# Performance work log

Hardware: AMD Instinct MI355X
Metric: run time of the kernel (lower is better)

The kernel has to match this reference:

```python
import jax, jax.numpy as jnp
import numpy as np

NHEAD = 8
HB, WB = 16, 16  # block_size


def _mha(q, k, v, w_in, b_in, w_out, b_out, nhead):
    # q,k,v: [L, B, C] seq-first, like torch.nn.MultiheadAttention (eval mode, no dropout)
    Lq, B, C = q.shape
    d = C // nhead
    wq, wk, wv = jnp.split(w_in, 3, axis=0)
    bq, bk, bv = jnp.split(b_in, 3)
    qh = (q @ wq.T + bq).reshape(Lq, B, nhead, d).transpose(1, 2, 0, 3)        # [B,H,Lq,d]
    kh = (k @ wk.T + bk).reshape(k.shape[0], B, nhead, d).transpose(1, 2, 0, 3)
    vh = (v @ wv.T + bv).reshape(v.shape[0], B, nhead, d).transpose(1, 2, 0, 3)
    scale = 1.0 / jnp.sqrt(jnp.asarray(d, dtype=qh.dtype))
    scores = jnp.einsum('bhqd,bhkd->bhqk', qh * scale, kh)
    attn = jax.nn.softmax(scores, axis=-1)
    out = jnp.einsum('bhqk,bhkd->bhqd', attn, vh)                               # [B,H,Lq,d]
    out = out.transpose(2, 0, 1, 3).reshape(Lq, B, C)
    return out @ w_out.T + b_out


def setup_inputs() -> dict:
    key = jax.random.key(0)
    ks = jax.random.split(key, 12)
    n, c, t, h, w = 2, 256, 2, 64, 64
    q = jax.random.normal(ks[0], (n, c, t, h, w), dtype=jnp.float32)
    k = jax.random.normal(ks[1], (n, c, t, h, w), dtype=jnp.float32)
    v = jax.random.normal(ks[2], (n, c, t, h, w), dtype=jnp.float32)
    pos = jax.random.normal(ks[3], (n, c, t, h, w), dtype=jnp.float32)
    s = 0.02
    wl_in = jax.random.normal(ks[4], (3 * c, c), dtype=jnp.float32) * s
    bl_in = jnp.zeros((3 * c,), dtype=jnp.float32)
    wl_out = jax.random.normal(ks[5], (c, c), dtype=jnp.float32) * s
    bl_out = jnp.zeros((c,), dtype=jnp.float32)
    ws_in = jax.random.normal(ks[6], (3 * c, c), dtype=jnp.float32) * s
    bs_in = jnp.zeros((3 * c,), dtype=jnp.float32)
    ws_out = jax.random.normal(ks[7], (c, c), dtype=jnp.float32) * s
    bs_out = jnp.zeros((c,), dtype=jnp.float32)
    return {"q": q, "k": k, "v": v, "pos": pos,
            "wl_in": wl_in, "bl_in": bl_in, "wl_out": wl_out, "bl_out": bl_out,
            "ws_in": ws_in, "bs_in": bs_in, "ws_out": ws_out, "bs_out": bs_out}


def reference(q, k, v, pos, wl_in, bl_in, wl_out, bl_out, ws_in, bs_in, ws_out, bs_out):
    n, c, t_q, h, w = q.shape
    t_k = k.shape[2]
    bn_h, bn_w = h // HB, w // WB

    def to_long(x, t):
        # [n,c,t,h,w] -> [t*bn_h*bn_w, n*HB*WB, c]
        x = x.reshape(n, c, t, bn_h, HB, bn_w, WB).transpose(2, 3, 5, 0, 4, 6, 1)
        return x.reshape(t * bn_h * bn_w, n * HB * WB, c)

    ql = to_long(q, t_q)
    kl = to_long(k, t_k)
    vl = to_long(v, t_k)
    pl = to_long(pos, t_q)

    v1 = _mha(ql + pl, kl + pl, vl, wl_in, bl_in, wl_out, bl_out, NHEAD)

    def long_to_short(x):
        # [t*bn_h*bn_w, n*HB*WB, c] -> [t*HB*WB, n*bn_h*bn_w, c]
        x = x.reshape(t_q, bn_h, bn_w, n, HB, WB, c).transpose(0, 4, 5, 3, 1, 2, 6)
        return x.reshape(t_q * HB * WB, n * bn_h * bn_w, c)

    v2 = long_to_short(v1)
    ps = long_to_short(pl)

    out = _mha(v2 + ps, v2 + ps, v2, ws_in, bs_in, ws_out, bs_out, NHEAD)
    out = out.reshape(t_q, HB, WB, n, bn_h, bn_w, c).transpose(3, 6, 0, 4, 1, 5, 2)
    return out.reshape(n, c, t_q, h, w)
```

## Files before the change

kernel.cpp:

```cpp
#include <hip/hip_runtime.h>
#include <math.h>


#define SCALE_D32 0.17677669529663687f
#define EXP2_SCALE 0.25508680987930193f
#define GLOBAL_AS __attribute__((address_space(1)))
#define LDS_AS __attribute__((address_space(3)))

typedef short short8 __attribute__((ext_vector_type(8)));
typedef short short4v __attribute__((ext_vector_type(4)));
typedef short short2v __attribute__((ext_vector_type(2)));
typedef float floatx4 __attribute__((ext_vector_type(4)));

__device__ __forceinline__ short f2bf(float f) {
  union { float f; unsigned u; } x;
  x.f = f;
  unsigned r = x.u + 0x7fffu + ((x.u >> 16) & 1u);
  return (short)(r >> 16);
}
__device__ __forceinline__ float bf2f(short s) {
  union { unsigned u; float f; } x;
  x.u = ((unsigned)(unsigned short)s) << 16;
  return x.f;
}

__global__ __launch_bounds__(256) void pack_kernel(
    const float* __restrict__ q, const float* __restrict__ k,
    const float* __restrict__ v, const float* __restrict__ pos,
    short* __restrict__ Xp, short* __restrict__ Xq,
    short* __restrict__ Xk, short* __restrict__ Xv,
    const float* __restrict__ wl_in, const float* __restrict__ wl_out,
    const float* __restrict__ ws_in, const float* __restrict__ ws_out,
    short* __restrict__ wbf) {
  __shared__ float tP[64][65];
  __shared__ float tX[64][65];
  int b = blockIdx.x;
  int cb = b & 3;
  int h  = (b >> 2) & 63;
  int nt = b >> 8;
  int n = nt >> 1, t = nt & 1;
  int c0 = cb * 64;
  int bh = h >> 4, ii = h & 15;
  long inbase = (long)n * 2097152 + (long)t * 4096 + (long)h * 64;
  int tx = threadIdx.x & 63;
  int ty = threadIdx.x >> 6;

  for (int cc = ty; cc < 64; cc += 4) {
    long a = inbase + (long)(c0 + cc) * 8192 + tx;
    tP[cc][tx] = pos[a];
    tX[cc][tx] = q[a];
  }
  __syncthreads();
  for (int ww = ty; ww < 64; ww += 4) {
    int bw = ww >> 4, j = ww & 15;
    int m1 = (((t * 4 + bh) * 4 + bw) * 512) + n * 256 + ii * 16 + j;
    long o = (long)m1 * 256 + c0 + tx;
    float pv = tP[tx][ww];
    Xp[o] = f2bf(pv);
    Xq[o] = f2bf(tX[tx][ww] + pv);
  }
  __syncthreads();
  for (int cc = ty; cc < 64; cc += 4) {
    long a = inbase + (long)(c0 + cc) * 8192 + tx;
    tX[cc][tx] = k[a];
  }
  __syncthreads();
  for (int ww = ty; ww < 64; ww += 4) {
    int bw = ww >> 4, j = ww & 15;
    int m1 = (((t * 4 + bh) * 4 + bw) * 512) + n * 256 + ii * 16 + j;
    long o = (long)m1 * 256 + c0 + tx;
    Xk[o] = f2bf(tX[tx][ww] + tP[tx][ww]);
  }
  __syncthreads();
  for (int cc = ty; cc < 64; cc += 4) {
    long a = inbase + (long)(c0 + cc) * 8192 + tx;
    tX[cc][tx] = v[a];
  }
  __syncthreads();
  for (int ww = ty; ww < 64; ww += 4) {
    int bw = ww >> 4, j = ww & 15;
    int m1 = (((t * 4 + bh) * 4 + bw) * 512) + n * 256 + ii * 16 + j;
    long o = (long)m1 * 256 + c0 + tx;
    Xv[o] = f2bf(tX[tx][ww]);
  }
  int idx = (blockIdx.x * 256 + threadIdx.x) * 2;
  const float* wp;
  if (idx < 196608) wp = wl_in + idx;
  else if (idx < 262144) wp = wl_out + (idx - 196608);
  else if (idx < 458752) wp = ws_in + (idx - 262144);
  else wp = ws_out + (idx - 458752);
  float2 wv = *(const float2*)wp;
  wbf[idx] = f2bf(wv.x);
  wbf[idx + 1] = f2bf(wv.y);
}

template <bool OUT32>
__global__ __launch_bounds__(256) void gemm_tri(
    const short* __restrict__ A0, const short* __restrict__ A1,
    const short* __restrict__ A2, const short* __restrict__ W0,
    const float* __restrict__ bias0, void* __restrict__ C0,
    void* __restrict__ C1, void* __restrict__ C2) {
  __shared__ short As[128 * 64];
  __shared__ short Ws[64 * 64];
  int z = blockIdx.z;
  const short* A = (z == 0) ? A0 : ((z == 1) ? A1 : A2);
  const short* Wb = W0 + z * 65536;
  const float* bias = bias0 + z * 256;
  void* Csel = (z == 0) ? C0 : ((z == 1) ? C1 : C2);
  int m0 = blockIdx.x * 128;
  int n0 = blockIdx.y * 64;
  int tid = threadIdx.x;
  int lane = tid & 63, wave = tid >> 6;
  int wm = wave >> 1, wn = wave & 1;
  int l15 = lane & 15, quad = lane >> 4;
  int x7 = l15 & 7;
  int rsub = lane >> 3;
  int csub = lane & 7;

  floatx4 acc[4][2];
#pragma unroll
  for (int mt = 0; mt < 4; ++mt)
#pragma unroll
    for (int nt = 0; nt < 2; ++nt) acc[mt][nt] = (floatx4)(0.f);

  for (int kb = 0; kb < 4; ++kb) {
    int k0 = kb * 64;
    if (kb) __syncthreads();
#pragma unroll
    for (int j = 0; j < 4; ++j) {
      int r0 = (wave * 4 + j) * 8;
      int row = r0 + rsub;
      int c = csub ^ (row & 7);
      const short* gp = A + (long)(m0 + row) * 256 + k0 + c * 8;
      short* lp = &As[r0 * 64 + lane * 8];
      __builtin_amdgcn_global_load_lds((const GLOBAL_AS void*)gp,
                                       (LDS_AS void*)lp, 16, 0, 0);
    }
#pragma unroll
    for (int j = 0; j < 2; ++j) {
      int r0 = (wave * 2 + j) * 8;
      int row = r0 + rsub;
      int c = csub ^ (row & 7);
      const short* gp = Wb + (long)(n0 + row) * 256 + k0 + c * 8;
      short* lp = &Ws[r0 * 64 + lane * 8];
      __builtin_amdgcn_global_load_lds((const GLOBAL_AS void*)gp,
                                       (LDS_AS void*)lp, 16, 0, 0);
    }
    __syncthreads();
#pragma unroll
    for (int ks = 0; ks < 2; ++ks) {
      int pc = (ks * 4 + quad) ^ x7;
      short8 af[4], bfr[2];
#pragma unroll
      for (int mt = 0; mt < 4; ++mt) {
        int row = wm * 64 + mt * 16 + l15;
        af[mt] = *(const short8*)&As[row * 64 + pc * 8];
      }
#pragma unroll
      for (int nt = 0; nt < 2; ++nt) {
        int row = wn * 32 + nt * 16 + l15;
        bfr[nt] = *(const short8*)&Ws[row * 64 + pc * 8];
      }
#pragma unroll
      for (int mt = 0; mt < 4; ++mt)
#pragma unroll
        for (int nt = 0; nt < 2; ++nt)
          acc[mt][nt] = __builtin_amdgcn_mfma_f32_16x16x32_bf16(
              af[mt], bfr[nt], acc[mt][nt], 0, 0, 0);
    }
  }
  float bia0 = bias[n0 + wn * 32 + l15];
  float bia1 = bias[n0 + wn * 32 + 16 + l15];
#pragma unroll
  for (int mt = 0; mt < 4; ++mt) {
#pragma unroll
    for (int r = 0; r < 4; ++r) {
      int row = m0 + wm * 64 + mt * 16 + quad * 4 + r;
      long base = (long)row * 256 + n0 + wn * 32 + l15;
      if (OUT32) {
        float* C = (float*)Csel;
        C[base] = acc[mt][0][r] + bia0;
        C[base + 16] = acc[mt][1][r] + bia1;
      } else {
        short* C = (short*)Csel;
        C[base] = f2bf(acc[mt][0][r] + bia0);
        C[base + 16] = f2bf(acc[mt][1][r] + bia1);
      }
    }
  }
}

__global__ __launch_bounds__(256) void attn1_mfma(
    const short* __restrict__ Q1, const short* __restrict__ K1,
    const short* __restrict__ V1, short* __restrict__ O1) {
  __shared__ short Vs[32][264];
  __shared__ short Vt[4][32][40];
  __shared__ short Pw[4][32][40];
  int b1 = blockIdx.x;
  int tid = threadIdx.x;
  int wave = tid >> 6, lane = tid & 63;
  int l15 = lane & 15, quad = lane >> 4;

#pragma unroll
  for (int p = 0; p < 4; ++p) {
    int idx = p * 256 + tid;
    int row = idx >> 5;
    int c8 = idx & 31;
    *(short8*)&Vs[row][c8 * 8] =
        *(const short8*)(V1 + ((long)row * 512 + b1) * 256 + c8 * 8);
  }
  __syncthreads();

  int key = lane & 31;
  int dh = (lane >> 5) * 16;
  int pc = 2 * (key & 15) + (key >> 4);

#pragma unroll
  for (int h2 = 0; h2 < 2; ++h2) {
    int hh = wave * 2 + h2;
    long fbase = ((long)l15 * 512 + b1) * 256 + hh * 32 + quad * 8;
    short8 qf0 = *(const short8*)(Q1 + fbase);
    short8 qf1 = *(const short8*)(Q1 + fbase + 16 * 512 * 256);
    short8 kf0 = *(const short8*)(K1 + fbase);
    short8 kf1 = *(const short8*)(K1 + fbase + 16 * 512 * 256);
    short8 v0 = *(const short8*)&Vs[key][hh * 32 + dh];
    short8 v1 = *(const short8*)&Vs[key][hh * 32 + dh + 8];
#pragma unroll
    for (int j = 0; j < 8; ++j) {
      Vt[wave][dh + j][pc] = v0[j];
      Vt[wave][dh + 8 + j][pc] = v1[j];
    }
    floatx4 s00 = __builtin_amdgcn_mfma_f32_16x16x32_bf16(qf0, kf0, (floatx4)(0.f), 0, 0, 0);
    floatx4 s01 = __builtin_amdgcn_mfma_f32_16x16x32_bf16(qf0, kf1, (floatx4)(0.f), 0, 0, 0);
    floatx4 s10 = __builtin_amdgcn_mfma_f32_16x16x32_bf16(qf1, kf0, (floatx4)(0.f), 0, 0, 0);
    floatx4 s11 = __builtin_amdgcn_mfma_f32_16x16x32_bf16(qf1, kf1, (floatx4)(0.f), 0, 0, 0);
    float li0[4], li1[4];
#pragma unroll
    for (int r = 0; r < 4; ++r) {
      float p00 = __builtin_amdgcn_exp2f(s00[r] * EXP2_SCALE);
      float p01 = __builtin_amdgcn_exp2f(s01[r] * EXP2_SCALE);
      float p10 = __builtin_amdgcn_exp2f(s10[r] * EXP2_SCALE);
      float p11 = __builtin_amdgcn_exp2f(s11[r] * EXP2_SCALE);
      li0[r] = p00 + p01;
      li1[r] = p10 + p11;
      short2v pa, pb;
      pa.x = f2bf(p00); pa.y = f2bf(p01);
      pb.x = f2bf(p10); pb.y = f2bf(p11);
      *(short2v*)&Pw[wave][quad * 4 + r][2 * l15] = pa;
      *(short2v*)&Pw[wave][16 + quad * 4 + r][2 * l15] = pb;
    }
#pragma unroll
    for (int r = 0; r < 4; ++r) {
      li0[r] += __shfl_xor(li0[r], 1, 64);
      li0[r] += __shfl_xor(li0[r], 2, 64);
      li0[r] += __shfl_xor(li0[r], 4, 64);
      li0[r] += __shfl_xor(li0[r], 8, 64);
      li1[r] += __shfl_xor(li1[r], 1, 64);
      li1[r] += __shfl_xor(li1[r], 2, 64);
      li1[r] += __shfl_xor(li1[r], 4, 64);
      li1[r] += __shfl_xor(li1[r], 8, 64);
    }
    short8 pf0 = *(const short8*)&Pw[wave][l15][quad * 8];
    short8 pf1 = *(const short8*)&Pw[wave][16 + l15][quad * 8];
    short8 vt0 = *(const short8*)&Vt[wave][l15][quad * 8];
    short8 vt1 = *(const short8*)&Vt[wave][16 + l15][quad * 8];
    floatx4 o00 = __builtin_amdgcn_mfma_f32_16x16x32_bf16(pf0, vt0, (floatx4)(0.f), 0, 0, 0);
    floatx4 o01 = __builtin_amdgcn_mfma_f32_16x16x32_bf16(pf0, vt1, (floatx4)(0.f), 0, 0, 0);
    floatx4 o10 = __builtin_amdgcn_mfma_f32_16x16x32_bf16(pf1, vt0, (floatx4)(0.f), 0, 0, 0);
    floatx4 o11 = __builtin_amdgcn_mfma_f32_16x16x32_bf16(pf1, vt1, (floatx4)(0.f), 0, 0, 0);
#pragma unroll
    for (int r = 0; r < 4; ++r) {
      float inv0 = 1.f / li0[r];
      float inv1 = 1.f / li1[r];
      long oa = ((long)(quad * 4 + r) * 512 + b1) * 256 + hh * 32 + l15;
      long ob = ((long)(16 + quad * 4 + r) * 512 + b1) * 256 + hh * 32 + l15;
      O1[oa] = f2bf(o00[r] * inv0);
      O1[oa + 16] = f2bf(o01[r] * inv0);
      O1[ob] = f2bf(o10[r] * inv1);
      O1[ob + 16] = f2bf(o11[r] * inv1);
    }
  }
}

__global__ __launch_bounds__(256) void attn2_mfma(
    const short* __restrict__ Q2, const short* __restrict__ K2,
    const short* __restrict__ V2, short* __restrict__ O2) {
  __shared__ short Ks[64][40];
  __shared__ short Vt[32][72];
  __shared__ short Pw[4][16][72];
  int bid = blockIdx.x;
  int rest = bid & 255;
  int qblk = bid >> 8;
  int hh = 2 * (rest & 3) + (rest >> 7);
  int b2 = (rest >> 2) & 31;
  int tid = threadIdx.x;
  int wave = tid >> 6, lane = tid & 63;
  int l15 = lane & 15, quad = lane >> 4;

  short8 qf;
  {
    long tok = (long)(qblk * 64 + wave * 16 + l15) * 32 + b2;
    qf = *(const short8*)(Q2 + tok * 256 + hh * 32 + quad * 8);
  }
  floatx4 Oa = (floatx4)(0.f), Ob = (floatx4)(0.f);
  float li[4] = {0.f, 0.f, 0.f, 0.f};

  int skey = tid >> 2;
  int sd0 = (tid & 3) * 8;
  int vkey = lane;
  int vd0 = wave * 8;
  int vcol = (vkey & 15) * 4 + (vkey >> 4);

  for (int kb = 0; kb < 8; ++kb) {
    if (kb) __syncthreads();
    {
      long tok = (long)(kb * 64 + skey) * 32 + b2;
      *(short8*)&Ks[skey][sd0] = *(const short8*)(K2 + tok * 256 + hh * 32 + sd0);
    }
    {
      long tok = (long)(kb * 64 + vkey) * 32 + b2;
      short8 v = *(const short8*)(V2 + tok * 256 + hh * 32 + vd0);
#pragma unroll
      for (int j = 0; j < 8; ++j) Vt[vd0 + j][vcol] = v[j];
    }
    __syncthreads();
    floatx4 st[4];
#pragma unroll
    for (int kt = 0; kt < 4; ++kt) {
      short8 kf = *(const short8*)&Ks[kt * 16 + l15][quad * 8];
      st[kt] = __builtin_amdgcn_mfma_f32_16x16x32_bf16(qf, kf, (floatx4)(0.f), 0, 0, 0);
    }
#pragma unroll
    for (int r = 0; r < 4; ++r) {
      float p0 = __builtin_amdgcn_exp2f(st[0][r] * EXP2_SCALE);
      float p1 = __builtin_amdgcn_exp2f(st[1][r] * EXP2_SCALE);
      float p2 = __builtin_amdgcn_exp2f(st[2][r] * EXP2_SCALE);
      float p3 = __builtin_amdgcn_exp2f(st[3][r] * EXP2_SCALE);
      li[r] += (p0 + p1) + (p2 + p3);
      short4v pp;
      pp.x = f2bf(p0); pp.y = f2bf(p1); pp.z = f2bf(p2); pp.w = f2bf(p3);
      *(short4v*)&Pw[wave][quad * 4 + r][l15 * 4] = pp;
    }
#pragma unroll
    for (int kk = 0; kk < 2; ++kk) {
      short8 pf = *(const short8*)&Pw[wave][l15][kk * 32 + quad * 8];
      short8 v0 = *(const short8*)&Vt[l15][kk * 32 + quad * 8];
      short8 v1 = *(const short8*)&Vt[16 + l15][kk * 32 + quad * 8];
      Oa = __builtin_amdgcn_mfma_f32_16x16x32_bf16(pf, v0, Oa, 0, 0, 0);
      Ob = __builtin_amdgcn_mfma_f32_16x16x32_bf16(pf, v1, Ob, 0, 0, 0);
    }
  }
#pragma unroll
  for (int r = 0; r < 4; ++r) {
    float s = li[r];
    s += __shfl_xor(s, 1, 64);
    s += __shfl_xor(s, 2, 64);
    s += __shfl_xor(s, 4, 64);
    s += __shfl_xor(s, 8, 64);
    float inv = 1.f / s;
    long tok = (long)(qblk * 64 + wave * 16 + quad * 4 + r) * 32 + b2;
    long a = tok * 256 + hh * 32 + l15;
    O2[a] = f2bf(Oa[r] * inv);
    O2[a + 16] = f2bf(Ob[r] * inv);
  }
}

__global__ __launch_bounds__(256) void perm12_kernel(
    const short8* __restrict__ V1o, const short8* __restrict__ Xp,
    short8* __restrict__ X2, short8* __restrict__ V2in) {
  int gg = blockIdx.x * 256 + threadIdx.x;
  int m1 = gg >> 5, seg = gg & 31;
  int l1 = m1 >> 9, b1 = m1 & 511;
  int t = l1 >> 4, bh = (l1 >> 2) & 3, bw = l1 & 3;
  int n = b1 >> 8, ii = (b1 >> 4) & 15, j = b1 & 15;
  int l2 = t * 256 + ii * 16 + j;
  int b2 = n * 16 + bh * 4 + bw;
  int m2 = l2 * 32 + b2;
  short8 v = V1o[gg];
  short8 p = Xp[gg];
  short8 x;
#pragma unroll
  for (int jj = 0; jj < 8; ++jj) x[jj] = f2bf(bf2f(v[jj]) + bf2f(p[jj]));
  X2[m2 * 32 + seg] = x;
  V2in[m2 * 32 + seg] = v;
}

__global__ __launch_bounds__(256) void unpack_kernel(
    const float* __restrict__ Y, float* __restrict__ out) {
  __shared__ float tl[64][65];
  int b = blockIdx.x;
  int cb = b & 3;
  int h = (b >> 2) & 63;
  int nt = b >> 8;
  int n = nt >> 1, t = nt & 1;
  int c0 = cb * 64;
  int bh = h >> 4, ii = h & 15;
  int tx = threadIdx.x & 63;
  int ty = threadIdx.x >> 6;
  for (int ww = ty; ww < 64; ww += 4) {
    int bw = ww >> 4, j = ww & 15;
    int l2 = t * 256 + ii * 16 + j;
    int b2 = n * 16 + bh * 4 + bw;
    int m2 = l2 * 32 + b2;
    tl[tx][ww] = Y[(long)m2 * 256 + c0 + tx];
  }
  __syncthreads();
  long ob = (long)n * 2097152 + (long)t * 4096 + (long)h * 64 + tx;
  for (int cc = ty; cc < 64; cc += 4) {
    out[ob + (long)(c0 + cc) * 8192] = tl[cc][tx];
  }
}

extern "C" void kernel_launch(void* const* d_in, const int* in_sizes, int n_in,
                              void* d_out, int out_size, void* d_ws, size_t ws_size,
                              hipStream_t stream) {
  const float* q      = (const float*)d_in[0];
  const float* k      = (const float*)d_in[1];
  const float* v      = (const float*)d_in[2];
  const float* pos    = (const float*)d_in[3];
  const float* wl_in  = (const float*)d_in[4];
  const float* bl_in  = (const float*)d_in[5];
  const float* wl_out = (const float*)d_in[6];
  const float* bl_out = (const float*)d_in[7];
  const float* ws_in  = (const float*)d_in[8];
  const float* bs_in  = (const float*)d_in[9];
  const float* ws_out = (const float*)d_in[10];
  const float* bs_out = (const float*)d_in[11];
  float* out = (float*)d_out;
  char* wsb = (char*)d_ws;
  const size_t SLB = 16777216;
  short* s0 = (short*)(wsb);
  short* wbf = (short*)(wsb + SLB / 2);
  short* s1 = (short*)(wsb + SLB);
  short* s2 = (short*)(wsb + 2 * SLB);
  short* s3 = (short*)(wsb + 3 * SLB);
  short* s4 = (short*)(wsb + 4 * SLB);
  short* s5 = (short*)(wsb + 5 * SLB);
  short* s6 = (short*)(wsb + 6 * SLB);

  pack_kernel<<<1024, 256, 0, stream>>>(q, k, v, pos, s0, s1, s2, s3,
                                        wl_in, wl_out, ws_in, ws_out, wbf);

  dim3 g3(128, 4, 3);
  dim3 g1(128, 4, 1);
  gemm_tri<false><<<g3, 256, 0, stream>>>(s1, s2, s3, wbf, bl_in, s4, s5, s6);

  attn1_mfma<<<512, 256, 0, stream>>>(s4, s5, s6, s1);
  gemm_tri<false><<<g1, 256, 0, stream>>>(s1, s1, s1, wbf + 196608, bl_out,
                                          s2, s2, s2);

  perm12_kernel<<<2048, 256, 0, stream>>>((const short8*)s2, (const short8*)s0,
                                          (short8*)s3, (short8*)s4);

  gemm_tri<false><<<g3, 256, 0, stream>>>(s3, s3, s4, wbf + 262144, bs_in,
                                          s5, s6, s1);

  attn2_mfma<<<2048, 256, 0, stream>>>(s5, s6, s1, s3);
  gemm_tri<true><<<g1, 256, 0, stream>>>(s3, s3, s3, wbf + 458752, bs_out,
                                         s2, s2, s2);

  unpack_kernel<<<1024, 256, 0, stream>>>((const float*)s2, out);
}
```

Baseline: 221.4 us.

## Fuse first attention, its output projection and the long-to-short permute

The first attention kernel now keeps each block's 32x256 output tile in swizzled LDS and multiplies it by the out-projection weights, which are streamed into LDS with global_load_lds. It adds bias and pos and writes X2 and V2in straight into the short-sequence layout. This removes a GEMM launch, the permute kernel and two intermediate round trips through global memory. In exchange, each block redundantly reloads the full 256x256 weight matrix, the kernel uses more LDS, and the epilogue stores are scattered 2-byte writes rather than vectorised ones.

```diff
diff --git a/kernel.cpp b/kernel.cpp
--- a/kernel.cpp
+++ b/kernel.cpp
@@ -22,6 +22,10 @@
   union { unsigned u; float f; } x;
   x.u = ((unsigned)(unsigned short)s) << 16;
   return x.f;
+}
+
+__device__ __forceinline__ int o1s_phys(int q, int ch) {
+  return q * 256 + (ch & ~63) + ((((ch >> 3) & 7) ^ (q & 7)) << 3) + (ch & 7);
 }
 
 __global__ __launch_bounds__(256) void pack_kernel(
@@ -190,30 +194,46 @@
   }
 }
 
-__global__ __launch_bounds__(256) void attn1_mfma(
+__global__ __launch_bounds__(256) void attn1_fused(
     const short* __restrict__ Q1, const short* __restrict__ K1,
-    const short* __restrict__ V1, short* __restrict__ O1) {
-  __shared__ short Vs[32][264];
-  __shared__ short Vt[4][32][40];
-  __shared__ short Pw[4][32][40];
+    const short* __restrict__ V1, const short* __restrict__ Xp,
+    const short* __restrict__ Wo, const float* __restrict__ bias,
+    short* __restrict__ X2, short* __restrict__ V2in) {
+  __shared__ union {
+    struct {
+      short Vs[32][264];
+      short Vt[4][32][40];
+      short Pw[4][32][40];
+    } a;
+    struct {
+      short O1s[32 * 256];
+      short Ws[256 * 64];
+    } g;
+  } u;
   int b1 = blockIdx.x;
   int tid = threadIdx.x;
   int wave = tid >> 6, lane = tid & 63;
   int l15 = lane & 15, quad = lane >> 4;
+  int x7 = l15 & 7;
+  int rsub = lane >> 3;
+  int csub = lane & 7;
 
 #pragma unroll
   for (int p = 0; p < 4; ++p) {
     int idx = p * 256 + tid;
     int row = idx >> 5;
     int c8 = idx & 31;
-    *(short8*)&Vs[row][c8 * 8] =
+    *(short8*)&u.a.Vs[row][c8 * 8] =
         *(const short8*)(V1 + ((long)row * 512 + b1) * 256 + c8 * 8);
   }
   __syncthreads();
 
   int key = lane & 31;
   int dh = (lane >> 5) * 16;
-  int pc = 2 * (key & 15) + (key >> 4);
+  int pc2 = 2 * (key & 15) + (key >> 4);
+
+  floatx4 oacc[2][4];
+  float lsum[2][2][4];
 
 #pragma unroll
   for (int h2 = 0; h2 < 2; ++h2) {
@@ -223,12 +243,12 @@
     short8 qf1 = *(const short8*)(Q1 + fbase + 16 * 512 * 256);
     short8 kf0 = *(const short8*)(K1 + fbase);
     short8 kf1 = *(const short8*)(K1 + fbase + 16 * 512 * 256);
-    short8 v0 = *(const short8*)&Vs[key][hh * 32 + dh];
-    short8 v1 = *(const short8*)&Vs[key][hh * 32 + dh + 8];
+    short8 v0 = *(const short8*)&u.a.Vs[key][hh * 32 + dh];
+    short8 v1 = *(const short8*)&u.a.Vs[key][hh * 32 + dh + 8];
 #pragma unroll
     for (int j = 0; j < 8; ++j) {
-      Vt[wave][dh + j][pc] = v0[j];
-      Vt[wave][dh + 8 + j][pc] = v1[j];
+      u.a.Vt[wave][dh + j][pc2] = v0[j];
+      u.a.Vt[wave][dh + 8 + j][pc2] = v1[j];
     }
     floatx4 s00 = __builtin_amdgcn_mfma_f32_16x16x32_bf16(qf0, kf0, (floatx4)(0.f), 0, 0, 0);
     floatx4 s01 = __builtin_amdgcn_mfma_f32_16x16x32_bf16(qf0, kf1, (floatx4)(0.f), 0, 0, 0);
@@ -246,8 +266,8 @@
       short2v pa, pb;
       pa.x = f2bf(p00); pa.y = f2bf(p01);
       pb.x = f2bf(p10); pb.y = f2bf(p11);
-      *(short2v*)&Pw[wave][quad * 4 + r][2 * l15] = pa;
-      *(short2v*)&Pw[wave][16 + quad * 4 + r][2 * l15] = pb;
+      *(short2v*)&u.a.Pw[wave][quad * 4 + r][2 * l15] = pa;
+      *(short2v*)&u.a.Pw[wave][16 + quad * 4 + r][2 * l15] = pb;
     }
 #pragma unroll
     for (int r = 0; r < 4; ++r) {
@@ -259,25 +279,96 @@
       li1[r] += __shfl_xor(li1[r], 2, 64);
       li1[r] += __shfl_xor(li1[r], 4, 64);
       li1[r] += __shfl_xor(li1[r], 8, 64);
-    }
-    short8 pf0 = *(const short8*)&Pw[wave][l15][quad * 8];
-    short8 pf1 = *(const short8*)&Pw[wave][16 + l15][quad * 8];
-    short8 vt0 = *(const short8*)&Vt[wave][l15][quad * 8];
-    short8 vt1 = *(const short8*)&Vt[wave][16 + l15][quad * 8];
-    floatx4 o00 = __builtin_amdgcn_mfma_f32_16x16x32_bf16(pf0, vt0, (floatx4)(0.f), 0, 0, 0);
-    floatx4 o01 = __builtin_amdgcn_mfma_f32_16x16x32_bf16(pf0, vt1, (floatx4)(0.f), 0, 0, 0);
-    floatx4 o10 = __builtin_amdgcn_mfma_f32_16x16x32_bf16(pf1, vt0, (floatx4)(0.f), 0, 0, 0);
-    floatx4 o11 = __builtin_amdgcn_mfma_f32_16x16x32_bf16(pf1, vt1, (floatx4)(0.f), 0, 0, 0);
+      lsum[h2][0][r] = li0[r];
+      lsum[h2][1][r] = li1[r];
+    }
+    short8 pf0 = *(const short8*)&u.a.Pw[wave][l15][quad * 8];
+    short8 pf1 = *(const short8*)&u.a.Pw[wave][16 + l15][quad * 8];
+    short8 vt0 = *(const short8*)&u.a.Vt[wave][l15][quad * 8];
+    short8 vt1 = *(const short8*)&u.a.Vt[wave][16 + l15][quad * 8];
+    oacc[h2][0] = __builtin_amdgcn_mfma_f32_16x16x32_bf16(pf0, vt0, (floatx4)(0.f), 0, 0, 0);
+    oacc[h2][1] = __builtin_amdgcn_mfma_f32_16x16x32_bf16(pf0, vt1, (floatx4)(0.f), 0, 0, 0);
+    oacc[h2][2] = __builtin_amdgcn_mfma_f32_16x16x32_bf16(pf1, vt0, (floatx4)(0.f), 0, 0, 0);
+    oacc[h2][3] = __builtin_amdgcn_mfma_f32_16x16x32_bf16(pf1, vt1, (floatx4)(0.f), 0, 0, 0);
+  }
+
+  __syncthreads();
+
+#pragma unroll
+  for (int h2 = 0; h2 < 2; ++h2) {
+    int hh = wave * 2 + h2;
+    int cA = hh * 32 + l15;
+    int cB = cA + 16;
 #pragma unroll
     for (int r = 0; r < 4; ++r) {
-      float inv0 = 1.f / li0[r];
-      float inv1 = 1.f / li1[r];
-      long oa = ((long)(quad * 4 + r) * 512 + b1) * 256 + hh * 32 + l15;
-      long ob = ((long)(16 + quad * 4 + r) * 512 + b1) * 256 + hh * 32 + l15;
-      O1[oa] = f2bf(o00[r] * inv0);
-      O1[oa + 16] = f2bf(o01[r] * inv0);
-      O1[ob] = f2bf(o10[r] * inv1);
-      O1[ob + 16] = f2bf(o11[r] * inv1);
+      float inv0 = 1.f / lsum[h2][0][r];
+      float inv1 = 1.f / lsum[h2][1][r];
+      int qa = quad * 4 + r, qb = 16 + quad * 4 + r;
+      u.g.O1s[o1s_phys(qa, cA)] = f2bf(oacc[h2][0][r] * inv0);
+      u.g.O1s[o1s_phys(qa, cB)] = f2bf(oacc[h2][1][r] * inv0);
+      u.g.O1s[o1s_phys(qb, cA)] = f2bf(oacc[h2][2][r] * inv1);
+      u.g.O1s[o1s_phys(qb, cB)] = f2bf(oacc[h2][3][r] * inv1);
+    }
+  }
+
+  floatx4 acc[2][4];
+#pragma unroll
+  for (int mt = 0; mt < 2; ++mt)
+#pragma unroll
+    for (int nt = 0; nt < 4; ++nt) acc[mt][nt] = (floatx4)(0.f);
+
+  for (int kb = 0; kb < 4; ++kb) {
+    __syncthreads();
+#pragma unroll
+    for (int j = 0; j < 8; ++j) {
+      int r0 = (wave * 8 + j) * 8;
+      int row = r0 + rsub;
+      int c = csub ^ (row & 7);
+      const short* gp = Wo + (long)row * 256 + kb * 64 + c * 8;
+      short* lp = &u.g.Ws[r0 * 64 + lane * 8];
+      __builtin_amdgcn_global_load_lds((const GLOBAL_AS void*)gp,
+                                       (LDS_AS void*)lp, 16, 0, 0);
+    }
+    __syncthreads();
+#pragma unroll
+    for (int ks = 0; ks < 2; ++ks) {
+      int pc = (ks * 4 + quad) ^ x7;
+      short8 af[2], bfr[4];
+#pragma unroll
+      for (int mt = 0; mt < 2; ++mt)
+        af[mt] = *(const short8*)&u.g.O1s[(mt * 16 + l15) * 256 + kb * 64 + pc * 8];
+#pragma unroll
+      for (int nt = 0; nt < 4; ++nt)
+        bfr[nt] = *(const short8*)&u.g.Ws[(wave * 64 + nt * 16 + l15) * 64 + pc * 8];
+#pragma unroll
+      for (int mt = 0; mt < 2; ++mt)
+#pragma unroll
+        for (int nt = 0; nt < 4; ++nt)
+          acc[mt][nt] = __builtin_amdgcn_mfma_f32_16x16x32_bf16(
+              af[mt], bfr[nt], acc[mt][nt], 0, 0, 0);
+    }
+  }
+
+  int nn = b1 >> 8, ii = (b1 >> 4) & 15, jj = b1 & 15;
+  float bv[4];
+#pragma unroll
+  for (int nt = 0; nt < 4; ++nt) bv[nt] = bias[wave * 64 + nt * 16 + l15];
+#pragma unroll
+  for (int mt = 0; mt < 2; ++mt) {
+#pragma unroll
+    for (int r = 0; r < 4; ++r) {
+      int qrow = mt * 16 + quad * 4 + r;
+      int t = qrow >> 4, bh = (qrow >> 2) & 3, bw = qrow & 3;
+      int m2 = (t * 256 + ii * 16 + jj) * 32 + nn * 16 + bh * 4 + bw;
+      long xbase = (long)m2 * 256;
+      long pbase = ((long)qrow * 512 + b1) * 256;
+#pragma unroll
+      for (int nt = 0; nt < 4; ++nt) {
+        int col = wave * 64 + nt * 16 + l15;
+        float val = acc[mt][nt][r] + bv[nt];
+        X2[xbase + col] = f2bf(val + bf2f(Xp[pbase + col]));
+        V2in[xbase + col] = f2bf(val);
+      }
     }
   }
 }
@@ -363,26 +454,6 @@
     O2[a] = f2bf(Oa[r] * inv);
     O2[a + 16] = f2bf(Ob[r] * inv);
   }
-}
-
-__global__ __launch_bounds__(256) void perm12_kernel(
-    const short8* __restrict__ V1o, const short8* __restrict__ Xp,
-    short8* __restrict__ X2, short8* __restrict__ V2in) {
-  int gg = blockIdx.x * 256 + threadIdx.x;
-  int m1 = gg >> 5, seg = gg & 31;
-  int l1 = m1 >> 9, b1 = m1 & 511;
-  int t = l1 >> 4, bh = (l1 >> 2) & 3, bw = l1 & 3;
-  int n = b1 >> 8, ii = (b1 >> 4) & 15, j = b1 & 15;
-  int l2 = t * 256 + ii * 16 + j;
-  int b2 = n * 16 + bh * 4 + bw;
-  int m2 = l2 * 32 + b2;
-  short8 v = V1o[gg];
-  short8 p = Xp[gg];
-  short8 x;
-#pragma unroll
-  for (int jj = 0; jj < 8; ++jj) x[jj] = f2bf(bf2f(v[jj]) + bf2f(p[jj]));
-  X2[m2 * 32 + seg] = x;
-  V2in[m2 * 32 + seg] = v;
 }
 
 __global__ __launch_bounds__(256) void unpack_kernel(
@@ -445,14 +516,10 @@
   dim3 g1(128, 4, 1);
   gemm_tri<false><<<g3, 256, 0, stream>>>(s1, s2, s3, wbf, bl_in, s4, s5, s6);
 
-  attn1_mfma<<<512, 256, 0, stream>>>(s4, s5, s6, s1);
-  gemm_tri<false><<<g1, 256, 0, stream>>>(s1, s1, s1, wbf + 196608, bl_out,
-                                          s2, s2, s2);
-
-  perm12_kernel<<<2048, 256, 0, stream>>>((const short8*)s2, (const short8*)s0,
-                                          (short8*)s3, (short8*)s4);
-
-  gemm_tri<false><<<g3, 256, 0, stream>>>(s3, s3, s4, wbf + 262144, bs_in,
+  attn1_fused<<<512, 256, 0, stream>>>(s4, s5, s6, s0, wbf + 196608, bl_out,
+                                       s3, s2);
+
+  gemm_tri<false><<<g3, 256, 0, stream>>>(s3, s3, s2, wbf + 262144, bs_in,
                                           s5, s6, s1);
 
   attn2_mfma<<<2048, 256, 0, stream>>>(s5, s6, s1, s3);
```

Result: faster. 209.5 us (-5.4%).
